# Performance work log

Hardware: AMD Instinct MI355X
Metric: run time of the kernel (lower is better)

The kernel has to match this reference:

```python
import jax, jax.numpy as jnp
import numpy as np
from jax import lax

B, N, C_IN, H, W = 256, 64, 3, 8, 8
CH = [32, 64, 128]   # cnn channels per stage
D = 128              # fc / gnn width
OUT = 5
BN_EPS = 1e-5


def setup_inputs() -> dict:
    key = jax.random.key(0)
    ks = jax.random.split(key, 24)
    x = jax.random.normal(ks[0], (B, N, C_IN, H, W), jnp.float32)
    # sparse symmetric communication graph, no self loops (GCNConv adds them)
    a = jax.random.uniform(ks[1], (B, N, N)) < 0.15
    a = jnp.logical_or(a, jnp.swapaxes(a, 1, 2)).astype(jnp.float32)
    gso = a * (1.0 - jnp.eye(N, dtype=jnp.float32))

    def lin(k, o, i):
        return (jax.random.normal(k, (o, i), jnp.float32) / np.sqrt(i)).astype(jnp.float32)

    def conv(k, o, i):
        return (jax.random.normal(k, (o, i, 3, 3), jnp.float32) / np.sqrt(i * 9)).astype(jnp.float32)

    inp = {
        'x': x, 'gso': gso,
        'w_c1': conv(ks[2], CH[0], C_IN), 'b_c1': jnp.zeros((CH[0],), jnp.float32),
        'g_bn1': jnp.ones((CH[0],), jnp.float32), 'be_bn1': jnp.zeros((CH[0],), jnp.float32),
        'w_c2': conv(ks[3], CH[1], CH[0]), 'b_c2': jnp.zeros((CH[1],), jnp.float32),
        'g_bn2': jnp.ones((CH[1],), jnp.float32), 'be_bn2': jnp.zeros((CH[1],), jnp.float32),
        'w_c3': conv(ks[4], CH[2], CH[1]), 'b_c3': jnp.zeros((CH[2],), jnp.float32),
        'g_bn3': jnp.ones((CH[2],), jnp.float32), 'be_bn3': jnp.zeros((CH[2],), jnp.float32),
        'w_fc': lin(ks[5], D, CH[2]), 'b_fc': jnp.zeros((D,), jnp.float32),
        'w_g1': lin(ks[6], D, D), 'b_g1': jnp.zeros((D,), jnp.float32),
        'w_g2': lin(ks[7], D, D), 'b_g2': jnp.zeros((D,), jnp.float32),
        'w_out': lin(ks[8], OUT, D), 'b_out': jnp.zeros((OUT,), jnp.float32),
    }
    return inp


def _cnn_block(h, w, b, g, be):
    h = lax.conv_general_dilated(h, w, (1, 1), 'SAME',
                                 dimension_numbers=('NCHW', 'OIHW', 'NCHW'))
    h = h + b[None, :, None, None]
    # eval-mode BatchNorm2d with running_mean=0, running_var=1
    h = h * (g / jnp.sqrt(1.0 + BN_EPS))[None, :, None, None] + be[None, :, None, None]
    h = jax.nn.relu(h)
    h = lax.reduce_window(h, -jnp.inf, lax.max, (1, 1, 2, 2), (1, 1, 2, 2), 'VALID')
    return h


def _forward(x, gso, w_c1, b_c1, g_bn1, be_bn1, w_c2, b_c2, g_bn2, be_bn2,
             w_c3, b_c3, g_bn3, be_bn3, w_fc, b_fc, w_g1, b_g1, w_g2, b_g2,
             w_out, b_out):
    b, n = x.shape[0], x.shape[1]
    h = x.reshape(b * n, x.shape[2], x.shape[3], x.shape[4])  # vectorize agents
    h = _cnn_block(h, w_c1, b_c1, g_bn1, be_bn1)
    h = _cnn_block(h, w_c2, b_c2, g_bn2, be_bn2)
    h = _cnn_block(h, w_c3, b_c3, g_bn3, be_bn3)          # [B*N, CH2, 1, 1]
    h = h.reshape(b * n, -1)
    h = jax.nn.relu(h @ w_fc.T + b_fc)                    # [B*N, D]
    feat = h.reshape(b, n, -1)
    # GCNConv: add self loops (weight 1), symmetric normalization
    a1 = gso + jnp.eye(n, dtype=gso.dtype)
    dinv = lax.rsqrt(a1.sum(-1))                          # deg >= 1
    ahat = dinv[:, :, None] * a1 * dinv[:, None, :]       # [B, N, N]
    hg = jax.nn.relu(jnp.einsum('bij,bjf->bif', ahat, feat @ w_g1.T) + b_g1)
    hg = jax.nn.relu(jnp.einsum('bij,bjf->bif', ahat, hg @ w_g2.T) + b_g2)
    actions = hg @ w_out.T + b_out                        # [B, N, OUT]
    return actions


def reference(x, gso, w_c1, b_c1, g_bn1, be_bn1, w_c2, b_c2, g_bn2, be_bn2,
              w_c3, b_c3, g_bn3, be_bn3, w_fc, b_fc, w_g1, b_g1, w_g2, b_g2,
              w_out, b_out):
    return _forward(x, gso, w_c1, b_c1, g_bn1, be_bn1, w_c2, b_c2, g_bn2, be_bn2,
                    w_c3, b_c3, g_bn3, be_bn3, w_fc, b_fc, w_g1, b_g1, w_g2, b_g2,
                    w_out, b_out)
```

## Files before the change

### kernel.cpp

```cpp
#include <hip/hip_runtime.h>
#include <math.h>


typedef __attribute__((ext_vector_type(8))) short bf16x8;
typedef __attribute__((ext_vector_type(4))) float f32x4;

__device__ __forceinline__ short f2bf(float f) {
  union { float f; unsigned u; } v; v.f = f;
  unsigned r = v.u + 0x7fffu + ((v.u >> 16) & 1u);
  return (short)(r >> 16);
}
__device__ __forceinline__ float bf2f(unsigned short u) {
  union { unsigned u; float f; } v; v.u = ((unsigned)u) << 16;
  return v.f;
}

__global__ __launch_bounds__(256) void pack_all(
    const float* __restrict__ w_c1, const float* __restrict__ w_c2,
    const float* __restrict__ w_c3, const float* __restrict__ w_fc,
    const float* __restrict__ w_g1, const float* __restrict__ w_g2,
    short* __restrict__ B1, short* __restrict__ B2, short* __restrict__ B3,
    short* __restrict__ Wfc, short* __restrict__ Wg1, short* __restrict__ Wg2) {
  int idx = blockIdx.x * 256 + threadIdx.x;
  if (idx < 2048) {
    int oc = idx >> 6, k = idx & 63;
    int t = k >> 2, ic = k & 3;
    float v = (t < 9 && ic < 3) ? w_c1[(oc * 3 + ic) * 9 + t] : 0.0f;
    B1[idx] = f2bf(v);
  } else if (idx < 20480) {
    int i2 = idx - 2048;
    int oc = i2 / 288, r = i2 - oc * 288;
    int t = r >> 5, ic = r & 31;
    B2[i2] = f2bf(w_c2[(oc * 32 + ic) * 9 + t]);
  } else if (idx < 94208) {
    int i3 = idx - 20480;
    int oc = i3 / 576, r = i3 - oc * 576;
    int t = r >> 6, ic = r & 63;
    B3[i3] = f2bf(w_c3[(oc * 64 + ic) * 9 + t]);
  } else if (idx < 110592) {
    int i = idx - 94208; Wfc[i] = f2bf(w_fc[i]);
  } else if (idx < 126976) {
    int i = idx - 110592; Wg1[i] = f2bf(w_g1[i]);
  } else if (idx < 143360) {
    int i = idx - 126976; Wg2[i] = f2bf(w_g2[i]);
  }
}

__global__ __launch_bounds__(256) void conv1_mfma(
    const float* __restrict__ x, const short* __restrict__ B1,
    const float* __restrict__ bias, const float* __restrict__ g,
    const float* __restrict__ be, short* __restrict__ c1) {
  __shared__ short sx[8 * 400];
  const int tid = threadIdx.x;
  const int s0 = blockIdx.x * 8;
  for (int i = tid; i < 400; i += 256)
    *(uint4*)(sx + i * 8) = (uint4){0, 0, 0, 0};
  __syncthreads();
  for (int p = tid; p < 512; p += 256) {
    const int si = p >> 6, pix = p & 63;
    const int y = pix >> 3, xx2 = pix & 7;
    const float* xb = x + (s0 + si) * 192 + pix;
    ushort4 o;
    o.x = (unsigned short)f2bf(xb[0]);
    o.y = (unsigned short)f2bf(xb[64]);
    o.z = (unsigned short)f2bf(xb[128]);
    o.w = 0;
    *(ushort4*)(sx + si * 400 + ((y + 1) * 10 + xx2 + 1) * 4) = o;
  }
  __syncthreads();
  const int lane = tid & 63, w = tid >> 6;
  const int col = lane & 15, quad = lane >> 4;
  bf16x8 Bf[2][2];
#pragma unroll
  for (int nt = 0; nt < 2; ++nt)
#pragma unroll
    for (int ks = 0; ks < 2; ++ks)
      Bf[nt][ks] = *(const bf16x8*)(B1 + (nt * 16 + col) * 64 + ks * 32 + quad * 8);
  float Abn[2], Cbn[2];
#pragma unroll
  for (int nt = 0; nt < 2; ++nt) {
    int oc = nt * 16 + col;
    float a = g[oc] * rsqrtf(1.0f + 1e-5f);
    Abn[nt] = a;
    Cbn[nt] = fmaf(bias[oc], a, be[oc]);
  }
  const int t0 = 2 * quad, t1 = t0 + 1;
  const int ky0 = t0 / 3, kx0 = t0 - 3 * (t0 / 3);
  const int ky1 = t1 / 3, kx1 = t1 - 3 * (t1 / 3);
  const int m = lane & 15;
  const int pl = m >> 2, sub = m & 3;
  const int dy = sub >> 1, dx = sub & 1;
  const uint2 z2 = {0u, 0u};
#pragma unroll
  for (int sl = 0; sl < 2; ++sl) {
    const int si = w * 2 + sl;
    const int s = s0 + si;
    const short* xb = sx + si * 400;
#pragma unroll
    for (int tile = 0; tile < 4; ++tile) {
      const int pi = tile * 4 + pl;
      const int py = pi >> 2, px = pi & 3;
      const int cy = 2 * py + dy, cx = 2 * px + dx;
      union { bf16x8 v; uint2 u[2]; } a0, a1;
      a0.u[0] = *(const uint2*)(xb + ((cy + ky0) * 10 + cx + kx0) * 4);
      a0.u[1] = *(const uint2*)(xb + ((cy + ky1) * 10 + cx + kx1) * 4);
      uint2 u8 = *(const uint2*)(xb + ((cy + 2) * 10 + cx + 2) * 4);
      a1.u[0] = (quad == 0) ? u8 : z2;
      a1.u[1] = z2;
      f32x4 acc0 = {0, 0, 0, 0}, acc1 = {0, 0, 0, 0};
      acc0 = __builtin_amdgcn_mfma_f32_16x16x32_bf16(a0.v, Bf[0][0], acc0, 0, 0, 0);
      acc0 = __builtin_amdgcn_mfma_f32_16x16x32_bf16(a1.v, Bf[0][1], acc0, 0, 0, 0);
      acc1 = __builtin_amdgcn_mfma_f32_16x16x32_bf16(a0.v, Bf[1][0], acc1, 0, 0, 0);
      acc1 = __builtin_amdgcn_mfma_f32_16x16x32_bf16(a1.v, Bf[1][1], acc1, 0, 0, 0);
      const int piq = tile * 4 + quad;
#pragma unroll
      for (int nt = 0; nt < 2; ++nt) {
        f32x4 acc = nt ? acc1 : acc0;
        float p0 = fmaf(acc[0], Abn[nt], Cbn[nt]);
        float p1 = fmaf(acc[1], Abn[nt], Cbn[nt]);
        float p2 = fmaf(acc[2], Abn[nt], Cbn[nt]);
        float p3 = fmaf(acc[3], Abn[nt], Cbn[nt]);
        float mx = fmaxf(fmaxf(fmaxf(p0, p1), fmaxf(p2, p3)), 0.0f);
        c1[s * 512 + piq * 32 + nt * 16 + col] = f2bf(mx);
      }
    }
  }
}

__global__ __launch_bounds__(256, 2) void conv2_mfma(
    const short* __restrict__ c1, const short* __restrict__ B2,
    const float* __restrict__ bias, const float* __restrict__ g,
    const float* __restrict__ be, short* __restrict__ c2) {
  const int lane = threadIdx.x & 63;
  const int wid = blockIdx.x * 4 + (threadIdx.x >> 6);
  const int col = lane & 15, quad = lane >> 4;
  bf16x8 Bf[4][9];
#pragma unroll
  for (int nt = 0; nt < 4; ++nt)
#pragma unroll
    for (int t = 0; t < 9; ++t)
      Bf[nt][t] = *(const bf16x8*)(B2 + (nt * 16 + col) * 288 + t * 32 + quad * 8);
  float Abn[4], Cbn[4];
#pragma unroll
  for (int nt = 0; nt < 4; ++nt) {
    int oc = nt * 16 + col;
    float a = g[oc] * rsqrtf(1.0f + 1e-5f);
    Abn[nt] = a;
    Cbn[nt] = fmaf(bias[oc], a, be[oc]);
  }
  const int m = lane & 15;
  const int q2 = m >> 2, sub = m & 3;
  const int cy = 2 * (q2 >> 1) + (sub >> 1);
  const int cx = 2 * (q2 & 1) + (sub & 1);
  int off[9];
  bool valid[9];
#pragma unroll
  for (int t = 0; t < 9; ++t) {
    int ky = t / 3, kx = t - 3 * (t / 3);
    int yy = cy + ky - 1, xx = cx + kx - 1;
    valid[t] = ((unsigned)yy < 4u) && ((unsigned)xx < 4u);
    int yc = min(max(yy, 0), 3), xc = min(max(xx, 0), 3);
    off[t] = (yc * 4 + xc) * 32 + quad * 8;
  }
  const bf16x8 zf = {0, 0, 0, 0, 0, 0, 0, 0};
#pragma unroll 1
  for (int si = 0; si < 8; ++si) {
    const int s = wid * 8 + si;
    const short* ib = c1 + s * 512;
    f32x4 acc[4];
#pragma unroll
    for (int nt = 0; nt < 4; ++nt) acc[nt] = (f32x4){0, 0, 0, 0};
#pragma unroll
    for (int t = 0; t < 9; ++t) {
      bf16x8 a = *(const bf16x8*)(ib + off[t]);
      if (!valid[t]) a = zf;
#pragma unroll
      for (int nt = 0; nt < 4; ++nt)
        acc[nt] = __builtin_amdgcn_mfma_f32_16x16x32_bf16(a, Bf[nt][t], acc[nt], 0, 0, 0);
    }
    short* ob = c2 + s * 256;
#pragma unroll
    for (int nt = 0; nt < 4; ++nt) {
      float p0 = fmaf(acc[nt][0], Abn[nt], Cbn[nt]);
      float p1 = fmaf(acc[nt][1], Abn[nt], Cbn[nt]);
      float p2 = fmaf(acc[nt][2], Abn[nt], Cbn[nt]);
      float p3 = fmaf(acc[nt][3], Abn[nt], Cbn[nt]);
      float mx = fmaxf(fmaxf(fmaxf(p0, p1), fmaxf(p2, p3)), 0.0f);
      ob[quad * 64 + nt * 16 + col] = f2bf(mx);
    }
  }
}

__global__ __launch_bounds__(256) void conv3_mfma(
    const short* __restrict__ c2, const short* __restrict__ B3,
    const float* __restrict__ bias, const float* __restrict__ g,
    const float* __restrict__ be, short* __restrict__ c3) {
  __shared__ short sB[32 * 584];
  const int tid = threadIdx.x;
  const int lane = tid & 63, w = tid >> 6;
  const int col = lane & 15, quad = lane >> 4;
  const int m = lane & 15;
  const int cp = m & 3, sl = m >> 2;
  const int cy = cp >> 1, cx = cp & 1;
  const int s = blockIdx.x * 16 + w * 4 + sl;
  const short* ib = c2 + s * 256;
  bf16x8 A[18];
  const bf16x8 zf = {0, 0, 0, 0, 0, 0, 0, 0};
#pragma unroll
  for (int ks = 0; ks < 18; ++ks) {
    int t = ks >> 1;
    int ky = t / 3, kx = t - 3 * (t / 3);
    int iy = cy + ky - 1, ix = cx + kx - 1;
    bool valid = ((unsigned)iy < 2u) && ((unsigned)ix < 2u);
    int iyc = min(max(iy, 0), 1), ixc = min(max(ix, 0), 1);
    bf16x8 a = *(const bf16x8*)(ib + (iyc * 2 + ixc) * 64 + (ks & 1) * 32 + quad * 8);
    A[ks] = valid ? a : zf;
  }
  f32x4 acc[8];
#pragma unroll
  for (int i = 0; i < 8; ++i) acc[i] = (f32x4){0, 0, 0, 0};
#pragma unroll
  for (int ng = 0; ng < 4; ++ng) {
    __syncthreads();
#pragma unroll
    for (int it = 0; it < 9; ++it) {
      int cidx = it * 256 + tid;
      int row = cidx / 72, seg = cidx - row * 72;
      *(bf16x8*)(sB + row * 584 + seg * 8) =
          *(const bf16x8*)(B3 + (ng * 32 + row) * 576 + seg * 8);
    }
    __syncthreads();
#pragma unroll
    for (int nt = 0; nt < 2; ++nt) {
      const int nB = (nt * 16 + col) * 584 + quad * 8;
#pragma unroll
      for (int ks = 0; ks < 18; ++ks) {
        bf16x8 b = *(const bf16x8*)(sB + nB + ks * 32);
        acc[ng * 2 + nt] =
            __builtin_amdgcn_mfma_f32_16x16x32_bf16(A[ks], b, acc[ng * 2 + nt], 0, 0, 0);
      }
    }
  }
  const int sample = blockIdx.x * 16 + w * 4 + quad;
#pragma unroll
  for (int i = 0; i < 8; ++i) {
    int oc = (i >> 1) * 32 + (i & 1) * 16 + col;
    float a = g[oc] * rsqrtf(1.0f + 1e-5f);
    float cc = fmaf(bias[oc], a, be[oc]);
    float p0 = fmaf(acc[i][0], a, cc);
    float p1 = fmaf(acc[i][1], a, cc);
    float p2 = fmaf(acc[i][2], a, cc);
    float p3 = fmaf(acc[i][3], a, cc);
    float mx = fmaxf(fmaxf(fmaxf(p0, p1), fmaxf(p2, p3)), 0.0f);
    c3[sample * 128 + oc] = f2bf(mx);
  }
}

__global__ __launch_bounds__(256) void fused_dense(
    const short* __restrict__ c3, const float* __restrict__ gso,
    const short* __restrict__ Wfc, const short* __restrict__ Wg1,
    const short* __restrict__ Wg2, const float* __restrict__ b_fc,
    const float* __restrict__ b_g1, const float* __restrict__ b_g2,
    const float* __restrict__ w_o, const float* __restrict__ b_o,
    float* __restrict__ out) {
  __shared__ short sAct[64 * 136];
  __shared__ short sT[128 * 72];
  __shared__ short sAhat[64 * 72];
  __shared__ float sDinv[64];
  __shared__ float sWo[640];
  const int tid = threadIdx.x;
  const int b = blockIdx.x;
  float* sG = (float*)sT;
  for (int i = tid; i < 4096; i += 256) sG[i] = gso[b * 4096 + i];
  for (int i = tid; i < 640; i += 256) sWo[i] = w_o[i];
  __syncthreads();
  if (tid < 64) {
    float ssum = 1.0f;
    for (int j = 0; j < 64; ++j) ssum += sG[j * 64 + tid];
    sDinv[tid] = rsqrtf(ssum);
  }
  __syncthreads();
  for (int i = tid; i < 4096; i += 256) {
    int r = i >> 6, c = i & 63;
    float v = sDinv[r] * (sG[i] + (r == c ? 1.0f : 0.0f)) * sDinv[c];
    sAhat[r * 72 + c] = f2bf(v);
  }
  for (int i = tid; i < 1024; i += 256) {
    int r = i >> 4, seg = i & 15;
    *(bf16x8*)(sAct + r * 136 + seg * 8) =
        *(const bf16x8*)(c3 + (b * 64 + r) * 128 + seg * 8);
  }
  __syncthreads();
  const int lane = tid & 63, w = tid >> 6;
  const int col = lane & 15, quad = lane >> 4;
  const int arow = (w * 16 + col) * 136;
  const int crow0 = (w * 16 + quad * 4) * 136;
  bf16x8 A[4];
  f32x4 acc[8];

#pragma unroll
  for (int ks = 0; ks < 4; ++ks)
    A[ks] = *(const bf16x8*)(sAct + arow + ks * 32 + quad * 8);
  __syncthreads();
#pragma unroll
  for (int i = 0; i < 8; ++i) acc[i] = (f32x4){0, 0, 0, 0};
#pragma unroll
  for (int nt = 0; nt < 8; ++nt) {
    const int n = nt * 16 + col;
#pragma unroll
    for (int ks = 0; ks < 4; ++ks) {
      bf16x8 bb = *(const bf16x8*)(Wfc + n * 128 + ks * 32 + quad * 8);
      acc[nt] = __builtin_amdgcn_mfma_f32_16x16x32_bf16(A[ks], bb, acc[nt], 0, 0, 0);
    }
  }
#pragma unroll
  for (int nt = 0; nt < 8; ++nt) {
    const int n = nt * 16 + col;
    const float bv = b_fc[n];
#pragma unroll
    for (int reg = 0; reg < 4; ++reg)
      sAct[crow0 + reg * 136 + n] = f2bf(fmaxf(acc[nt][reg] + bv, 0.0f));
  }
  __syncthreads();

#pragma unroll
  for (int ks = 0; ks < 4; ++ks)
    A[ks] = *(const bf16x8*)(sAct + arow + ks * 32 + quad * 8);
#pragma unroll
  for (int i = 0; i < 8; ++i) acc[i] = (f32x4){0, 0, 0, 0};
#pragma unroll
  for (int nt = 0; nt < 8; ++nt) {
    const int n = nt * 16 + col;
#pragma unroll
    for (int ks = 0; ks < 4; ++ks) {
      bf16x8 bb = *(const bf16x8*)(Wg1 + n * 128 + ks * 32 + quad * 8);
      acc[nt] = __builtin_amdgcn_mfma_f32_16x16x32_bf16(A[ks], bb, acc[nt], 0, 0, 0);
    }
  }
#pragma unroll
  for (int nt = 0; nt < 8; ++nt) {
    const int n = nt * 16 + col;
    ushort4 pk;
    pk.x = (unsigned short)f2bf(acc[nt][0]);
    pk.y = (unsigned short)f2bf(acc[nt][1]);
    pk.z = (unsigned short)f2bf(acc[nt][2]);
    pk.w = (unsigned short)f2bf(acc[nt][3]);
    *(ushort4*)(sT + n * 72 + w * 16 + quad * 4) = pk;
  }
  __syncthreads();

  bf16x8 Ah[2];
#pragma unroll
  for (int ks = 0; ks < 2; ++ks)
    Ah[ks] = *(const bf16x8*)(sAhat + (w * 16 + col) * 72 + ks * 32 + quad * 8);
#pragma unroll
  for (int i = 0; i < 8; ++i) acc[i] = (f32x4){0, 0, 0, 0};
#pragma unroll
  for (int nt = 0; nt < 8; ++nt) {
    const int n = nt * 16 + col;
#pragma unroll
    for (int ks = 0; ks < 2; ++ks) {
      bf16x8 bb = *(const bf16x8*)(sT + n * 72 + ks * 32 + quad * 8);
      acc[nt] = __builtin_amdgcn_mfma_f32_16x16x32_bf16(Ah[ks], bb, acc[nt], 0, 0, 0);
    }
  }
#pragma unroll
  for (int nt = 0; nt < 8; ++nt) {
    const int n = nt * 16 + col;
    const float bv = b_g1[n];
#pragma unroll
    for (int reg = 0; reg < 4; ++reg)
      sAct[crow0 + reg * 136 + n] = f2bf(fmaxf(acc[nt][reg] + bv, 0.0f));
  }
  __syncthreads();

#pragma unroll
  for (int ks = 0; ks < 4; ++ks)
    A[ks] = *(const bf16x8*)(sAct + arow + ks * 32 + quad * 8);
#pragma unroll
  for (int i = 0; i < 8; ++i) acc[i] = (f32x4){0, 0, 0, 0};
#pragma unroll
  for (int nt = 0; nt < 8; ++nt) {
    const int n = nt * 16 + col;
#pragma unroll
    for (int ks = 0; ks < 4; ++ks) {
      bf16x8 bb = *(const bf16x8*)(Wg2 + n * 128 + ks * 32 + quad * 8);
      acc[nt] = __builtin_amdgcn_mfma_f32_16x16x32_bf16(A[ks], bb, acc[nt], 0, 0, 0);
    }
  }
#pragma unroll
  for (int nt = 0; nt < 8; ++nt) {
    const int n = nt * 16 + col;
    ushort4 pk;
    pk.x = (unsigned short)f2bf(acc[nt][0]);
    pk.y = (unsigned short)f2bf(acc[nt][1]);
    pk.z = (unsigned short)f2bf(acc[nt][2]);
    pk.w = (unsigned short)f2bf(acc[nt][3]);
    *(ushort4*)(sT + n * 72 + w * 16 + quad * 4) = pk;
  }
  __syncthreads();

#pragma unroll
  for (int i = 0; i < 8; ++i) acc[i] = (f32x4){0, 0, 0, 0};
#pragma unroll
  for (int nt = 0; nt < 8; ++nt) {
    const int n = nt * 16 + col;
#pragma unroll
    for (int ks = 0; ks < 2; ++ks) {
      bf16x8 bb = *(const bf16x8*)(sT + n * 72 + ks * 32 + quad * 8);
      acc[nt] = __builtin_amdgcn_mfma_f32_16x16x32_bf16(Ah[ks], bb, acc[nt], 0, 0, 0);
    }
  }
#pragma unroll
  for (int nt = 0; nt < 8; ++nt) {
    const int n = nt * 16 + col;
    const float bv = b_g2[n];
#pragma unroll
    for (int reg = 0; reg < 4; ++reg)
      sAct[crow0 + reg * 136 + n] = f2bf(fmaxf(acc[nt][reg] + bv, 0.0f));
  }
  __syncthreads();

  {
    const int j = tid >> 2, o = tid & 3;
    float a0 = 0.0f;
#pragma unroll
    for (int k8 = 0; k8 < 16; ++k8) {
      union { bf16x8 v; unsigned short u[8]; } h;
      h.v = *(const bf16x8*)(sAct + j * 136 + k8 * 8);
#pragma unroll
      for (int jj = 0; jj < 8; ++jj)
        a0 = fmaf(bf2f(h.u[jj]), sWo[o * 128 + k8 * 8 + jj], a0);
    }
    out[(b * 64 + j) * 5 + o] = a0 + b_o[o];
    if (tid < 64) {
      float a4 = 0.0f;
#pragma unroll
      for (int k8 = 0; k8 < 16; ++k8) {
        union { bf16x8 v; unsigned short u[8]; } h;
        h.v = *(const bf16x8*)(sAct + tid * 136 + k8 * 8);
#pragma unroll
        for (int jj = 0; jj < 8; ++jj)
          a4 = fmaf(bf2f(h.u[jj]), sWo[512 + k8 * 8 + jj], a4);
      }
      out[(b * 64 + tid) * 5 + 4] = a4 + b_o[4];
    }
  }
}

extern "C" void kernel_launch(void* const* d_in, const int* in_sizes, int n_in,
                              void* d_out, int out_size, void* d_ws, size_t ws_size,
                              hipStream_t stream) {
  const float* x    = (const float*)d_in[0];
  const float* gso  = (const float*)d_in[1];
  const float* w_c1 = (const float*)d_in[2];
  const float* b_c1 = (const float*)d_in[3];
  const float* g_b1 = (const float*)d_in[4];
  const float* e_b1 = (const float*)d_in[5];
  const float* w_c2 = (const float*)d_in[6];
  const float* b_c2 = (const float*)d_in[7];
  const float* g_b2 = (const float*)d_in[8];
  const float* e_b2 = (const float*)d_in[9];
  const float* w_c3 = (const float*)d_in[10];
  const float* b_c3 = (const float*)d_in[11];
  const float* g_b3 = (const float*)d_in[12];
  const float* e_b3 = (const float*)d_in[13];
  const float* w_fc = (const float*)d_in[14];
  const float* b_fc = (const float*)d_in[15];
  const float* w_g1 = (const float*)d_in[16];
  const float* b_g1 = (const float*)d_in[17];
  const float* w_g2 = (const float*)d_in[18];
  const float* b_g2 = (const float*)d_in[19];
  const float* w_o  = (const float*)d_in[20];
  const float* b_o  = (const float*)d_in[21];
  float* out = (float*)d_out;
  char* ws = (char*)d_ws;

  short* c1  = (short*)(ws + 0);
  short* c2  = (short*)(ws + 16777216);
  short* c3  = (short*)(ws + 25165824);
  short* B1  = (short*)(ws + 29360128);
  short* B2  = (short*)(ws + 29364224);
  short* B3  = (short*)(ws + 29401088);
  short* Wfc = (short*)(ws + 29548544);
  short* Wg1 = (short*)(ws + 29581312);
  short* Wg2 = (short*)(ws + 29614080);

  pack_all<<<560, 256, 0, stream>>>(w_c1, w_c2, w_c3, w_fc, w_g1, w_g2,
                                    B1, B2, B3, Wfc, Wg1, Wg2);
  conv1_mfma<<<2048, 256, 0, stream>>>(x, B1, b_c1, g_b1, e_b1, c1);
  conv2_mfma<<<512, 256, 0, stream>>>(c1, B2, b_c2, g_b2, e_b2, c2);
  conv3_mfma<<<1024, 256, 0, stream>>>(c2, B3, b_c3, g_b3, e_b3, c3);
  fused_dense<<<256, 256, 0, stream>>>(c3, gso, Wfc, Wg1, Wg2, b_fc, b_g1,
                                       b_g2, w_o, b_o, out);
}
```

Before: 176.7 us.

## Stage conv2/conv3 inputs through padded LDS and widen dense kernel to 512 threads

conv2 and conv3 now copy each block's input activations into LDS with coalesced 16-byte loads, using padded row strides, and read the im2col fragments from LDS instead of strided global gathers. fused_dense runs with 512 threads, so each of 8 waves handles half of the output columns, and the final 5-output projection is spread over 320 threads. This targets uncoalesced global reads and underused parallelism in the per-batch dense kernel. In exchange it adds LDS footprint and extra barriers, which may lower occupancy.

Result: slower. 181.1 us (+2.5%).

```diff
diff --git a/kernel.cpp b/kernel.cpp
--- a/kernel.cpp
+++ b/kernel.cpp
@@ -131,8 +131,18 @@
     const short* __restrict__ c1, const short* __restrict__ B2,
     const float* __restrict__ bias, const float* __restrict__ g,
     const float* __restrict__ be, short* __restrict__ c2) {
-  const int lane = threadIdx.x & 63;
-  const int wid = blockIdx.x * 4 + (threadIdx.x >> 6);
+  __shared__ short sx[32 * 640];
+  const int tid = threadIdx.x;
+  const int s0 = blockIdx.x * 32;
+#pragma unroll
+  for (int it = 0; it < 8; ++it) {
+    int c = it * 256 + tid;
+    int s_l = c >> 6, k = c & 63;
+    int cell = k >> 2, seg = k & 3;
+    *(bf16x8*)(sx + s_l * 640 + cell * 40 + seg * 8) =
+        *(const bf16x8*)(c1 + s0 * 512 + c * 8);
+  }
+  const int lane = tid & 63, w = tid >> 6;
   const int col = lane & 15, quad = lane >> 4;
   bf16x8 Bf[4][9];
 #pragma unroll
@@ -160,13 +170,14 @@
     int yy = cy + ky - 1, xx = cx + kx - 1;
     valid[t] = ((unsigned)yy < 4u) && ((unsigned)xx < 4u);
     int yc = min(max(yy, 0), 3), xc = min(max(xx, 0), 3);
-    off[t] = (yc * 4 + xc) * 32 + quad * 8;
+    off[t] = (yc * 4 + xc) * 40 + quad * 8;
   }
   const bf16x8 zf = {0, 0, 0, 0, 0, 0, 0, 0};
+  __syncthreads();
 #pragma unroll 1
   for (int si = 0; si < 8; ++si) {
-    const int s = wid * 8 + si;
-    const short* ib = c1 + s * 512;
+    const int s_l = w * 8 + si;
+    const short* ib = sx + s_l * 640;
     f32x4 acc[4];
 #pragma unroll
     for (int nt = 0; nt < 4; ++nt) acc[nt] = (f32x4){0, 0, 0, 0};
@@ -178,7 +189,7 @@
       for (int nt = 0; nt < 4; ++nt)
         acc[nt] = __builtin_amdgcn_mfma_f32_16x16x32_bf16(a, Bf[nt][t], acc[nt], 0, 0, 0);
     }
-    short* ob = c2 + s * 256;
+    short* ob = c2 + (s0 + s_l) * 256;
 #pragma unroll
     for (int nt = 0; nt < 4; ++nt) {
       float p0 = fmaf(acc[nt][0], Abn[nt], Cbn[nt]);
@@ -196,14 +207,24 @@
     const float* __restrict__ bias, const float* __restrict__ g,
     const float* __restrict__ be, short* __restrict__ c3) {
   __shared__ short sB[32 * 584];
+  __shared__ short sA[16 * 296];
   const int tid = threadIdx.x;
+  const int s0 = blockIdx.x * 16;
+#pragma unroll
+  for (int it = 0; it < 2; ++it) {
+    int c = it * 256 + tid;
+    int s_l = c >> 5, k = c & 31;
+    int cell = k >> 3, seg = k & 7;
+    *(bf16x8*)(sA + s_l * 296 + cell * 72 + seg * 8) =
+        *(const bf16x8*)(c2 + s0 * 256 + c * 8);
+  }
+  __syncthreads();
   const int lane = tid & 63, w = tid >> 6;
   const int col = lane & 15, quad = lane >> 4;
   const int m = lane & 15;
   const int cp = m & 3, sl = m >> 2;
   const int cy = cp >> 1, cx = cp & 1;
-  const int s = blockIdx.x * 16 + w * 4 + sl;
-  const short* ib = c2 + s * 256;
+  const short* ib = sA + (w * 4 + sl) * 296;
   bf16x8 A[18];
   const bf16x8 zf = {0, 0, 0, 0, 0, 0, 0, 0};
 #pragma unroll
@@ -213,7 +234,7 @@
     int iy = cy + ky - 1, ix = cx + kx - 1;
     bool valid = ((unsigned)iy < 2u) && ((unsigned)ix < 2u);
     int iyc = min(max(iy, 0), 1), ixc = min(max(ix, 0), 1);
-    bf16x8 a = *(const bf16x8*)(ib + (iyc * 2 + ixc) * 64 + (ks & 1) * 32 + quad * 8);
+    bf16x8 a = *(const bf16x8*)(ib + (iyc * 2 + ixc) * 72 + (ks & 1) * 32 + quad * 8);
     A[ks] = valid ? a : zf;
   }
   f32x4 acc[8];
@@ -241,7 +262,7 @@
       }
     }
   }
-  const int sample = blockIdx.x * 16 + w * 4 + quad;
+  const int sample = s0 + w * 4 + quad;
 #pragma unroll
   for (int i = 0; i < 8; ++i) {
     int oc = (i >> 1) * 32 + (i & 1) * 16 + col;
@@ -256,7 +277,7 @@
   }
 }
 
-__global__ __launch_bounds__(256) void fused_dense(
+__global__ __launch_bounds__(512) void fused_dense(
     const short* __restrict__ c3, const float* __restrict__ gso,
     const short* __restrict__ Wfc, const short* __restrict__ Wg1,
     const short* __restrict__ Wg2, const float* __restrict__ b_fc,
@@ -271,8 +292,8 @@
   const int tid = threadIdx.x;
   const int b = blockIdx.x;
   float* sG = (float*)sT;
-  for (int i = tid; i < 4096; i += 256) sG[i] = gso[b * 4096 + i];
-  for (int i = tid; i < 640; i += 256) sWo[i] = w_o[i];
+  for (int i = tid; i < 4096; i += 512) sG[i] = gso[b * 4096 + i];
+  for (int i = tid; i < 640; i += 512) sWo[i] = w_o[i];
   __syncthreads();
   if (tid < 64) {
     float ssum = 1.0f;
@@ -280,46 +301,47 @@
     sDinv[tid] = rsqrtf(ssum);
   }
   __syncthreads();
-  for (int i = tid; i < 4096; i += 256) {
+  for (int i = tid; i < 4096; i += 512) {
     int r = i >> 6, c = i & 63;
     float v = sDinv[r] * (sG[i] + (r == c ? 1.0f : 0.0f)) * sDinv[c];
     sAhat[r * 72 + c] = f2bf(v);
   }
-  for (int i = tid; i < 1024; i += 256) {
+  for (int i = tid; i < 1024; i += 512) {
     int r = i >> 4, seg = i & 15;
     *(bf16x8*)(sAct + r * 136 + seg * 8) =
         *(const bf16x8*)(c3 + (b * 64 + r) * 128 + seg * 8);
   }
   __syncthreads();
-  const int lane = tid & 63, w = tid >> 6;
+  const int lane = tid & 63, w8 = tid >> 6;
+  const int rg = w8 >> 1, nh = w8 & 1;
   const int col = lane & 15, quad = lane >> 4;
-  const int arow = (w * 16 + col) * 136;
-  const int crow0 = (w * 16 + quad * 4) * 136;
+  const int arow = (rg * 16 + col) * 136;
+  const int crow0 = (rg * 16 + quad * 4) * 136;
   bf16x8 A[4];
-  f32x4 acc[8];
+  f32x4 acc[4];
 
 #pragma unroll
   for (int ks = 0; ks < 4; ++ks)
     A[ks] = *(const bf16x8*)(sAct + arow + ks * 32 + quad * 8);
   __syncthreads();
 #pragma unroll
-  for (int i = 0; i < 8; ++i) acc[i] = (f32x4){0, 0, 0, 0};
-#pragma unroll
-  for (int nt = 0; nt < 8; ++nt) {
-    const int n = nt * 16 + col;
+  for (int i = 0; i < 4; ++i) acc[i] = (f32x4){0, 0, 0, 0};
+#pragma unroll
+  for (int ntl = 0; ntl < 4; ++ntl) {
+    const int n = (nh * 4 + ntl) * 16 + col;
 #pragma unroll
     for (int ks = 0; ks < 4; ++ks) {
       bf16x8 bb = *(const bf16x8*)(Wfc + n * 128 + ks * 32 + quad * 8);
-      acc[nt] = __builtin_amdgcn_mfma_f32_16x16x32_bf16(A[ks], bb, acc[nt], 0, 0, 0);
-    }
-  }
-#pragma unroll
-  for (int nt = 0; nt < 8; ++nt) {
-    const int n = nt * 16 + col;
+      acc[ntl] = __builtin_amdgcn_mfma_f32_16x16x32_bf16(A[ks], bb, acc[ntl], 0, 0, 0);
+    }
+  }
+#pragma unroll
+  for (int ntl = 0; ntl < 4; ++ntl) {
+    const int n = (nh * 4 + ntl) * 16 + col;
     const float bv = b_fc[n];
 #pragma unroll
     for (int reg = 0; reg < 4; ++reg)
-      sAct[crow0 + reg * 136 + n] = f2bf(fmaxf(acc[nt][reg] + bv, 0.0f));
+      sAct[crow0 + reg * 136 + n] = f2bf(fmaxf(acc[ntl][reg] + bv, 0.0f));
   }
   __syncthreads();
 
@@ -327,50 +349,50 @@
   for (int ks = 0; ks < 4; ++ks)
     A[ks] = *(const bf16x8*)(sAct + arow + ks * 32 + quad * 8);
 #pragma unroll
-  for (int i = 0; i < 8; ++i) acc[i] = (f32x4){0, 0, 0, 0};
-#pragma unroll
-  for (int nt = 0; nt < 8; ++nt) {
-    const int n = nt * 16 + col;
+  for (int i = 0; i < 4; ++i) acc[i] = (f32x4){0, 0, 0, 0};
+#pragma unroll
+  for (int ntl = 0; ntl < 4; ++ntl) {
+    const int n = (nh * 4 + ntl) * 16 + col;
 #pragma unroll
     for (int ks = 0; ks < 4; ++ks) {
       bf16x8 bb = *(const bf16x8*)(Wg1 + n * 128 + ks * 32 + quad * 8);
-      acc[nt] = __builtin_amdgcn_mfma_f32_16x16x32_bf16(A[ks], bb, acc[nt], 0, 0, 0);
-    }
-  }
-#pragma unroll
-  for (int nt = 0; nt < 8; ++nt) {
-    const int n = nt * 16 + col;
+      acc[ntl] = __builtin_amdgcn_mfma_f32_16x16x32_bf16(A[ks], bb, acc[ntl], 0, 0, 0);
+    }
+  }
+#pragma unroll
+  for (int ntl = 0; ntl < 4; ++ntl) {
+    const int n = (nh * 4 + ntl) * 16 + col;
     ushort4 pk;
-    pk.x = (unsigned short)f2bf(acc[nt][0]);
-    pk.y = (unsigned short)f2bf(acc[nt][1]);
-    pk.z = (unsigned short)f2bf(acc[nt][2]);
-    pk.w = (unsigned short)f2bf(acc[nt][3]);
-    *(ushort4*)(sT + n * 72 + w * 16 + quad * 4) = pk;
+    pk.x = (unsigned short)f2bf(acc[ntl][0]);
+    pk.y = (unsigned short)f2bf(acc[ntl][1]);
+    pk.z = (unsigned short)f2bf(acc[ntl][2]);
+    pk.w = (unsigned short)f2bf(acc[ntl][3]);
+    *(ushort4*)(sT + n * 72 + rg * 16 + quad * 4) = pk;
   }
   __syncthreads();
 
   bf16x8 Ah[2];
 #pragma unroll
   for (int ks = 0; ks < 2; ++ks)
-    Ah[ks] = *(const bf16x8*)(sAhat + (w * 16 + col) * 72 + ks * 32 + quad * 8);
-#pragma unroll
-  for (int i = 0; i < 8; ++i) acc[i] = (f32x4){0, 0, 0, 0};
-#pragma unroll
-  for (int nt = 0; nt < 8; ++nt) {
-    const int n = nt * 16 + col;
+    Ah[ks] = *(const bf16x8*)(sAhat + (rg * 16 + col) * 72 + ks * 32 + quad * 8);
+#pragma unroll
+  for (int i = 0; i < 4; ++i) acc[i] = (f32x4){0, 0, 0, 0};
+#pragma unroll
+  for (int ntl = 0; ntl < 4; ++ntl) {
+    const int n = (nh * 4 + ntl) * 16 + col;
 #pragma unroll
     for (int ks = 0; ks < 2; ++ks) {
       bf16x8 bb = *(const bf16x8*)(sT + n * 72 + ks * 32 + quad * 8);
-      acc[nt] = __builtin_amdgcn_mfma_f32_16x16x32_bf16(Ah[ks], bb, acc[nt], 0, 0, 0);
-    }
-  }
-#pragma unroll
-  for (int nt = 0; nt < 8; ++nt) {
-    const int n = nt * 16 + col;
+      acc[ntl] = __builtin_amdgcn_mfma_f32_16x16x32_bf16(Ah[ks], bb, acc[ntl], 0, 0, 0);
+    }
+  }
+#pragma unroll
+  for (int ntl = 0; ntl < 4; ++ntl) {
+    const int n = (nh * 4 + ntl) * 16 + col;
     const float bv = b_g1[n];
 #pragma unroll
     for (int reg = 0; reg < 4; ++reg)
-      sAct[crow0 + reg * 136 + n] = f2bf(fmaxf(acc[nt][reg] + bv, 0.0f));
+      sAct[crow0 + reg * 136 + n] = f2bf(fmaxf(acc[ntl][reg] + bv, 0.0f));
   }
   __syncthreads();
 
@@ -378,51 +400,51 @@
   for (int ks = 0; ks < 4; ++ks)
     A[ks] = *(const bf16x8*)(sAct + arow + ks * 32 + quad * 8);
 #pragma unroll
-  for (int i = 0; i < 8; ++i) acc[i] = (f32x4){0, 0, 0, 0};
-#pragma unroll
-  for (int nt = 0; nt < 8; ++nt) {
-    const int n = nt * 16 + col;
+  for (int i = 0; i < 4; ++i) acc[i] = (f32x4){0, 0, 0, 0};
+#pragma unroll
+  for (int ntl = 0; ntl < 4; ++ntl) {
+    const int n = (nh * 4 + ntl) * 16 + col;
 #pragma unroll
     for (int ks = 0; ks < 4; ++ks) {
       bf16x8 bb = *(const bf16x8*)(Wg2 + n * 128 + ks * 32 + quad * 8);
-      acc[nt] = __builtin_amdgcn_mfma_f32_16x16x32_bf16(A[ks], bb, acc[nt], 0, 0, 0);
-    }
-  }
-#pragma unroll
-  for (int nt = 0; nt < 8; ++nt) {
-    const int n = nt * 16 + col;
+      acc[ntl] = __builtin_amdgcn_mfma_f32_16x16x32_bf16(A[ks], bb, acc[ntl], 0, 0, 0);
+    }
+  }
+#pragma unroll
+  for (int ntl = 0; ntl < 4; ++ntl) {
+    const int n = (nh * 4 + ntl) * 16 + col;
     ushort4 pk;
-    pk.x = (unsigned short)f2bf(acc[nt][0]);
-    pk.y = (unsigned short)f2bf(acc[nt][1]);
-    pk.z = (unsigned short)f2bf(acc[nt][2]);
-    pk.w = (unsigned short)f2bf(acc[nt][3]);
-    *(ushort4*)(sT + n * 72 + w * 16 + quad * 4) = pk;
-  }
-  __syncthreads();
-
-#pragma unroll
-  for (int i = 0; i < 8; ++i) acc[i] = (f32x4){0, 0, 0, 0};
-#pragma unroll
-  for (int nt = 0; nt < 8; ++nt) {
-    const int n = nt * 16 + col;
+    pk.x = (unsigned short)f2bf(acc[ntl][0]);
+    pk.y = (unsigned short)f2bf(acc[ntl][1]);
+    pk.z = (unsigned short)f2bf(acc[ntl][2]);
+    pk.w = (unsigned short)f2bf(acc[ntl][3]);
+    *(ushort4*)(sT + n * 72 + rg * 16 + quad * 4) = pk;
+  }
+  __syncthreads();
+
+#pragma unroll
+  for (int i = 0; i < 4; ++i) acc[i] = (f32x4){0, 0, 0, 0};
+#pragma unroll
+  for (int ntl = 0; ntl < 4; ++ntl) {
+    const int n = (nh * 4 + ntl) * 16 + col;
 #pragma unroll
     for (int ks = 0; ks < 2; ++ks) {
       bf16x8 bb = *(const bf16x8*)(sT + n * 72 + ks * 32 + quad * 8);
-      acc[nt] = __builtin_amdgcn_mfma_f32_16x16x32_bf16(Ah[ks], bb, acc[nt], 0, 0, 0);
-    }
-  }
-#pragma unroll
-  for (int nt = 0; nt < 8; ++nt) {
-    const int n = nt * 16 + col;
+      acc[ntl] = __builtin_amdgcn_mfma_f32_16x16x32_bf16(Ah[ks], bb, acc[ntl], 0, 0, 0);
+    }
+  }
+#pragma unroll
+  for (int ntl = 0; ntl < 4; ++ntl) {
+    const int n = (nh * 4 + ntl) * 16 + col;
     const float bv = b_g2[n];
 #pragma unroll
     for (int reg = 0; reg < 4; ++reg)
-      sAct[crow0 + reg * 136 + n] = f2bf(fmaxf(acc[nt][reg] + bv, 0.0f));
-  }
-  __syncthreads();
-
-  {
-    const int j = tid >> 2, o = tid & 3;
+      sAct[crow0 + reg * 136 + n] = f2bf(fmaxf(acc[ntl][reg] + bv, 0.0f));
+  }
+  __syncthreads();
+
+  if (tid < 320) {
+    const int j = tid / 5, o = tid - 5 * j;
     float a0 = 0.0f;
 #pragma unroll
     for (int k8 = 0; k8 < 16; ++k8) {
@@ -433,18 +455,6 @@
         a0 = fmaf(bf2f(h.u[jj]), sWo[o * 128 + k8 * 8 + jj], a0);
     }
     out[(b * 64 + j) * 5 + o] = a0 + b_o[o];
-    if (tid < 64) {
-      float a4 = 0.0f;
-#pragma unroll
-      for (int k8 = 0; k8 < 16; ++k8) {
-        union { bf16x8 v; unsigned short u[8]; } h;
-        h.v = *(const bf16x8*)(sAct + tid * 136 + k8 * 8);
-#pragma unroll
-        for (int jj = 0; jj < 8; ++jj)
-          a4 = fmaf(bf2f(h.u[jj]), sWo[512 + k8 * 8 + jj], a4);
-      }
-      out[(b * 64 + tid) * 5 + 4] = a4 + b_o[4];
-    }
   }
 }
 
@@ -491,6 +501,6 @@
   conv1_mfma<<<2048, 256, 0, stream>>>(x, B1, b_c1, g_b1, e_b1, c1);
   conv2_mfma<<<512, 256, 0, stream>>>(c1, B2, b_c2, g_b2, e_b2, c2);
   conv3_mfma<<<1024, 256, 0, stream>>>(c2, B3, b_c3, g_b3, e_b3, c3);
-  fused_dense<<<256, 256, 0, stream>>>(c3, gso, Wfc, Wg1, Wg2, b_fc, b_g1,
+  fused_dense<<<256, 512, 0, stream>>>(c3, gso, Wfc, Wg1, Wg2, b_fc, b_g1,
                                        b_g2, w_o, b_o, out);
 }
```
